# Performance work log

Measured on AMD Instinct MI355X. Metric: run time of the kernel, lower is better.

The kernel has to match this reference:

```python
import jax, jax.numpy as jnp
import numpy as np

EMBED_DIM = 1024
HEADS = 16
HD = EMBED_DIM // HEADS

def setup_inputs() -> dict:
    key = jax.random.key(0)
    ks = jax.random.split(key, 6)
    s = 1.0 / np.sqrt(EMBED_DIM)
    x = jax.random.normal(ks[0], (4, 2048, EMBED_DIM), dtype=jnp.float32)
    Wq = jax.random.uniform(ks[1], (EMBED_DIM, EMBED_DIM), jnp.float32, -s, s)
    Wk = jax.random.uniform(ks[2], (EMBED_DIM, EMBED_DIM), jnp.float32, -s, s)
    Wv = jax.random.uniform(ks[3], (EMBED_DIM, EMBED_DIM), jnp.float32, -s, s)
    Wo = jax.random.uniform(ks[4], (EMBED_DIM, EMBED_DIM), jnp.float32, -s, s)
    bo = jax.random.uniform(ks[5], (EMBED_DIM,), jnp.float32, -s, s)
    return {"x": x, "Wq": Wq, "Wk": Wk, "Wv": Wv, "Wo": Wo, "bo": bo}

def reference(x, Wq, Wk, Wv, Wo, bo):
    B, S, E = x.shape
    # projections (torch Linear: y = x @ W.T), split into heads -> [B,H,S,hd]
    def proj(W):
        return (x @ W.T).reshape(B, S, HEADS, HD).transpose(0, 2, 1, 3)
    q, k, v = proj(Wq), proj(Wk), proj(Wv)
    energy = jnp.einsum('bhid,bhjd->bhij', q, k) / np.sqrt(HD).astype(np.float32)
    causal = jnp.tril(jnp.ones((S, S), dtype=bool))
    energy = jnp.where(causal, energy, -jnp.inf)
    attn = jax.nn.softmax(energy, axis=-1)  # dropout omitted (eval mode)
    out = jnp.einsum('bhij,bhjd->bhid', attn, v)
    out = out.transpose(0, 2, 1, 3).reshape(B, S, E)
    return out @ Wo.T + bo
```

## Files before the change

### kernel.cpp

```cpp
#include <hip/hip_runtime.h>
#include <math.h>

#define EMB   1024
#define HEADS 16
#define HD    64
#define SEQ   2048
#define BATCH 4
#define MTOT  (BATCH * SEQ)
#define XSZ   ((size_t)MTOT * EMB)
#define WSZ   ((size_t)EMB * EMB)

typedef __attribute__((ext_vector_type(8))) short s16x8;
typedef __attribute__((ext_vector_type(4))) short s16x4;
typedef __attribute__((ext_vector_type(4))) float f32x4;

__device__ __forceinline__ short f2bf(float f) {
    unsigned u = __builtin_bit_cast(unsigned, f);
    u += 0x7fffu + ((u >> 16) & 1u);
    return (short)(u >> 16);
}

__device__ __forceinline__ unsigned pk_bf16(float a, float b) {
#if __has_builtin(__builtin_amdgcn_cvt_pk_bf16_f32)
    typedef __attribute__((ext_vector_type(2))) __bf16 bf16x2;
    return __builtin_bit_cast(unsigned, __builtin_amdgcn_cvt_pk_bf16_f32(a, b));
#else
    return (unsigned)(unsigned short)f2bf(a) |
           ((unsigned)(unsigned short)f2bf(b) << 16);
#endif
}

__device__ __forceinline__ float fexp2(float x) {
#if __has_builtin(__builtin_amdgcn_exp2f)
    return __builtin_amdgcn_exp2f(x);
#else
    return exp2f(x);
#endif
}

__device__ __forceinline__ void async16(const void* g, void* l) {
    __builtin_amdgcn_global_load_lds(
        (const __attribute__((address_space(1))) unsigned*)g,
        (__attribute__((address_space(3))) unsigned*)l, 16, 0, 0);
}

__global__ __launch_bounds__(256)
void cvt_inputs(const float* __restrict__ x,  const float* __restrict__ wq,
                const float* __restrict__ wk, const float* __restrict__ wv,
                const float* __restrict__ wo, short* __restrict__ xb,
                short* __restrict__ wcat)
{
    const size_t e = ((size_t)blockIdx.x * 256 + threadIdx.x) * 8;
    const float* src;
    short* dst;
    float scale = 1.0f;
    if (e < XSZ) {
        src = x + e;
        dst = xb + e;
    } else {
        const size_t r = e - XSZ;
        const int w = (int)(r >> 20);
        const size_t off = r & (WSZ - 1);
        src = (w == 0 ? wq : w == 1 ? wk : w == 2 ? wv : wo) + off;
        dst = wcat + r;
        if (w == 0) scale = 0.125f * 1.44269504f;
    }
    const float4 a = ((const float4*)src)[0];
    const float4 b = ((const float4*)src)[1];
    s16x8 v;
    v[0] = f2bf(a.x * scale); v[1] = f2bf(a.y * scale);
    v[2] = f2bf(a.z * scale); v[3] = f2bf(a.w * scale);
    v[4] = f2bf(b.x * scale); v[5] = f2bf(b.y * scale);
    v[6] = f2bf(b.z * scale); v[7] = f2bf(b.w * scale);
    *(s16x8*)dst = v;
}

#define BAR() __builtin_amdgcn_s_barrier()
#define WAIT_LGKM() do { asm volatile("s_waitcnt lgkmcnt(0)" ::: "memory"); \
                         __builtin_amdgcn_sched_barrier(0); } while (0)
#define WAIT_VM(n) asm volatile("s_waitcnt vmcnt(" #n ")" ::: "memory")

#define RD_A4(bA) \
    _Pragma("unroll") for (int mi = 0; mi < 4; ++mi) \
    _Pragma("unroll") for (int kk = 0; kk < 2; ++kk) \
        a[mi][kk] = *(const s16x8*)((bA) + (wm4 + mi) * 2048 + kk * 1024 + abase);

#define RD_B2(bB, hf, breg) \
    _Pragma("unroll") for (int ni = 0; ni < 2; ++ni) \
    _Pragma("unroll") for (int kk = 0; kk < 2; ++kk) \
        breg[ni][kk] = *(const s16x8*)((bB) + (wn4 + (hf) * 2 + ni) * 2048 + kk * 1024 + abase);

#define MFMA16(hf, breg) \
    __builtin_amdgcn_s_setprio(1); \
    _Pragma("unroll") for (int mi = 0; mi < 4; ++mi) \
    _Pragma("unroll") for (int ni = 0; ni < 2; ++ni) \
    _Pragma("unroll") for (int kk = 0; kk < 2; ++kk) \
        acc[mi][(hf) * 2 + ni] = __builtin_amdgcn_mfma_f32_16x16x32_bf16( \
            a[mi][kk], breg[ni][kk], acc[mi][(hf) * 2 + ni], 0, 0, 0); \
    __builtin_amdgcn_s_setprio(0);

#define STA(pM, ldsM, h, k0) do { \
    async16((pM) + (size_t)((h) * 128) * K + (k0),      (ldsM) + (h) * 16384 + wv1024); \
    async16((pM) + (size_t)((h) * 128 + 64) * K + (k0), (ldsM) + (h) * 16384 + 8192 + wv1024); \
} while (0)

#define STB(pM, ldsM, k0) do { \
    async16((pM) + (k0),                (ldsM) + wv1024); \
    async16((pM) + (size_t)64 * K + (k0), (ldsM) + 8192 + wv1024); \
} while (0)

template<bool OUT_BF16>
__global__ __launch_bounds__(512, 2)
void gemm_qp(const short* __restrict__ A, const short* __restrict__ B,
             void* __restrict__ C, int ldc, const float* __restrict__ bias,
             int K)
{
    __shared__ __align__(16) char lds[147456];

    const int tid   = threadIdx.x;
    const int wv    = tid >> 6;
    const int lane  = tid & 63;
    const int col16 = lane & 15;
    const int quad  = lane >> 4;
    const int wm    = wv >> 1;
    const int wn    = wv & 1;
    const int wm4   = wm * 4;
    const int wn4   = wn * 4;
    const int wv1024 = wv << 10;

    const int nwg = gridDim.x * gridDim.y;
    int wg = blockIdx.y * gridDim.x + blockIdx.x;
    wg = (wg & 7) * (nwg >> 3) + (wg >> 3);
    const int rowBase = (wg / gridDim.x) * 256;
    const int colBase = (wg % gridDim.x) * 128;

    const int abase = (col16 * 64 + quad * 16) ^ ((col16 & 8) << 2);

    const int rlane = (lane >> 2) & 15;
    const int rw0   = ((wv >> 1) << 4) + rlane;
    const int colSt = ((wv & 1) << 5) + (((lane & 3) << 3) ^ ((lane & 32) >> 1));
    const short* pA = A + (size_t)(rowBase + rw0) * K + colSt;
    const short* pB = B + (size_t)(colBase + rw0) * K + colSt;

    s16x8 a[4][2], bq0[2][2], bq1[2][2];
    f32x4 acc[4][4];
#pragma unroll
    for (int i = 0; i < 4; ++i)
#pragma unroll
        for (int j = 0; j < 4; ++j) acc[i][j] = (f32x4){0.f, 0.f, 0.f, 0.f};

    const int NT = K >> 6;

    char* r0 = lds;
    char* r1 = lds + 49152;
    char* r2 = lds + 98304;

    STA(pA, r0, 0, 0);  STA(pA, r0, 1, 0);  STB(pB, r0 + 32768, 0);
    STA(pA, r1, 0, 64); STA(pA, r1, 1, 64); STB(pB, r1 + 32768, 64);
    WAIT_VM(6);
    BAR();

    for (int kt = 0; kt < NT; ++kt) {
        const int k0 = kt << 6;
        const bool more = (kt + 2 < NT);

        RD_A4(r0);
        RD_B2(r0 + 32768, 0, bq0);
        if (more) { STA(pA, r2, 0, k0 + 128); STB(pB, r2 + 32768, k0 + 128); }
        BAR(); WAIT_LGKM();
        MFMA16(0, bq0);
        BAR();

        RD_B2(r0 + 32768, 1, bq1);
        if (more) STA(pA, r2, 1, k0 + 128);
        BAR(); WAIT_LGKM();
        MFMA16(1, bq1);
        if (more) { WAIT_VM(6); } else { WAIT_VM(0); }
        BAR();

        char* t = r0; r0 = r1; r1 = r2; r2 = t;
    }

    if (OUT_BF16) {
        short* Cb = (short*)C;
#pragma unroll
        for (int mi = 0; mi < 4; ++mi) {
            const int rg0 = rowBase + wm * 64 + mi * 16 + quad * 4;
#pragma unroll
            for (int ni = 0; ni < 4; ++ni) {
                const int cg = colBase + wn * 64 + ni * 16 + col16;
                const f32x4 v = acc[mi][ni];
#pragma unroll
                for (int r = 0; r < 4; ++r)
                    Cb[(size_t)(rg0 + r) * ldc + cg] = f2bf(v[r]);
            }
        }
    } else {
        float* Cf = (float*)C;
#pragma unroll
        for (int ni = 0; ni < 4; ++ni) {
            const int cg = colBase + wn * 64 + ni * 16 + col16;
            const float bj = bias ? bias[cg] : 0.f;
#pragma unroll
            for (int mi = 0; mi < 4; ++mi) {
                const int rg0 = rowBase + wm * 64 + mi * 16 + quad * 4;
                const f32x4 v = acc[mi][ni];
#pragma unroll
                for (int r = 0; r < 4; ++r)
                    Cf[(size_t)(rg0 + r) * ldc + cg] = v[r] + bj;
            }
        }
    }
}

#define LDQ 3072
__global__ __launch_bounds__(512)
void attn_mfma(const short* __restrict__ QKV, short* __restrict__ O)
{
    __shared__ short lK[64 * 64];
    __shared__ short lV[64 * 64];
    __shared__ short lP[8 * 32 * 64];

    char* lKc = (char*)lK;
    char* lVc = (char*)lV;
    char* lPc = (char*)lP;

    const int tid  = threadIdx.x;
    const int wv   = tid >> 6;
    const int lane = tid & 63;
    const int col  = lane & 15;
    const int quad = lane >> 4;
    const int csw  = (col & 7) << 4;

    const int linear = (int)blockIdx.y * 8 + (int)blockIdx.x;
    const int hlf = linear >> 8;
    const int r9  = linear & 255;
    const int bh  = (hlf << 5) + (r9 >> 3);
    const int xr  = r9 & 7;
    const int qsuper = hlf ? (7 - xr) : xr;

    const int b  = bh >> 4;
    const int h  = bh & 15;
    const size_t baseq = (size_t)b * SEQ * LDQ + (size_t)h * HD;
    const size_t basek = baseq + 1024;
    const size_t basev = baseq + 2048;
    const size_t baseo = (size_t)b * SEQ * EMB + (size_t)h * HD;

    const int krow = tid >> 3;
    const int kwoff = krow * 128 + ((((tid & 7) * 16)) ^ ((krow & 7) << 4));
    char* pwv = lPc + wv * 4096;

    const s16x8 onesv = {0x3F80, 0x3F80, 0x3F80, 0x3F80,
                         0x3F80, 0x3F80, 0x3F80, 0x3F80};

    const int qb = qsuper * 256;
    const int qlo_w = qb + wv * 32;

    s16x8 qf[2][2];
#pragma unroll
    for (int rb = 0; rb < 2; ++rb) {
        const short* qr = QKV + baseq + (size_t)(qlo_w + rb * 16 + col) * LDQ;
        qf[rb][0] = *(const s16x8*)(qr + quad * 8);
        qf[rb][1] = *(const s16x8*)(qr + 32 + quad * 8);
    }

    f32x4 of[2][4], lsum[2];
#pragma unroll
    for (int rb = 0; rb < 2; ++rb) {
#pragma unroll
        for (int u = 0; u < 4; ++u) of[rb][u] = (f32x4){0.f, 0.f, 0.f, 0.f};
        lsum[rb] = (f32x4){0.f, 0.f, 0.f, 0.f};
    }

    const int nt = qb / 64 + 4;

    s16x8 pk = *(const s16x8*)(QKV + basek + (size_t)krow * LDQ + (tid & 7) * 8);
    s16x8 pv = *(const s16x8*)(QKV + basev + (size_t)lane * LDQ + wv * 8);

    for (int kt = 0; kt < nt; ++kt) {
        const int kb = kt * 64;
        __syncthreads();
        *(s16x8*)(lKc + kwoff) = pk;
#pragma unroll
        for (int t = 0; t < 8; ++t)
            *(short*)(lVc + (wv * 8 + t) * 128 + ((lane * 2) ^ (t << 4))) = pv[t];
        __syncthreads();

        if (kt + 1 < nt) {
            pk = *(const s16x8*)(QKV + basek + (size_t)(kb + 64 + krow) * LDQ + (tid & 7) * 8);
            pv = *(const s16x8*)(QKV + basev + (size_t)(kb + 64 + lane) * LDQ + wv * 8);
        }

        if (kb > qlo_w + 31) continue;

        s16x8 kf[4][2];
#pragma unroll
        for (int t = 0; t < 4; ++t) {
            kf[t][0] = *(const s16x8*)(lKc + (t * 16 + col) * 128 + ((quad * 16) ^ csw));
            kf[t][1] = *(const s16x8*)(lKc + (t * 16 + col) * 128 + ((64 + quad * 16) ^ csw));
        }

#pragma unroll
        for (int rb = 0; rb < 2; ++rb) {
            const int qlo = qlo_w + rb * 16;
            const int qg  = qlo + col;

            f32x4 s[4];
#pragma unroll
            for (int t = 0; t < 4; ++t) {
                f32x4 acc = (f32x4){0.f, 0.f, 0.f, 0.f};
                acc = __builtin_amdgcn_mfma_f32_16x16x32_bf16(kf[t][0], qf[rb][0], acc, 0, 0, 0);
                acc = __builtin_amdgcn_mfma_f32_16x16x32_bf16(kf[t][1], qf[rb][1], acc, 0, 0, 0);
                s[t] = acc;
            }

            if (kb + 63 > qlo) {
#pragma unroll
                for (int t = 0; t < 4; ++t)
#pragma unroll
                    for (int rr = 0; rr < 4; ++rr) {
                        const int kg = kb + t * 16 + quad * 4 + rr;
                        if (kg > qg) s[t][rr] = -3.0e38f;
                    }
            }

            char* pb = pwv + (rb * 16 + col) * 128;
#pragma unroll
            for (int t = 0; t < 4; ++t) {
                uint2 pkd;
                pkd.x = pk_bf16(fexp2(s[t][0]), fexp2(s[t][1]));
                pkd.y = pk_bf16(fexp2(s[t][2]), fexp2(s[t][3]));
                *(uint2*)(pb + ((t * 32 + quad * 8) ^ csw)) = pkd;
            }
        }

#pragma unroll
        for (int c = 0; c < 2; ++c) {
            s16x8 vf[4];
#pragma unroll
            for (int u = 0; u < 4; ++u)
                vf[u] = *(const s16x8*)(lVc + (u * 16 + col) * 128 + ((c * 64 + quad * 16) ^ csw));
#pragma unroll
            for (int rb = 0; rb < 2; ++rb) {
                const s16x8 pa = *(const s16x8*)(pwv + (rb * 16 + col) * 128 + ((c * 64 + quad * 16) ^ csw));
                lsum[rb] = __builtin_amdgcn_mfma_f32_16x16x32_bf16(onesv, pa, lsum[rb], 0, 0, 0);
#pragma unroll
                for (int u = 0; u < 4; ++u)
                    of[rb][u] = __builtin_amdgcn_mfma_f32_16x16x32_bf16(vf[u], pa, of[rb][u], 0, 0, 0);
            }
        }
    }

#pragma unroll
    for (int rb = 0; rb < 2; ++rb) {
        const float rl = 1.f / lsum[rb][0];
        short* orow = O + baseo + (size_t)(qlo_w + rb * 16 + col) * EMB + quad * 4;
#pragma unroll
        for (int u = 0; u < 4; ++u) {
            uint2 pkd;
            pkd.x = pk_bf16(of[rb][u][0] * rl, of[rb][u][1] * rl);
            pkd.y = pk_bf16(of[rb][u][2] * rl, of[rb][u][3] * rl);
            *(uint2*)&orow[u * 16] = pkd;
        }
    }
}

extern "C" void kernel_launch(void* const* d_in, const int* in_sizes, int n_in,
                              void* d_out, int out_size, void* d_ws, size_t ws_size,
                              hipStream_t stream)
{
    const float* x  = (const float*)d_in[0];
    const float* Wq = (const float*)d_in[1];
    const float* Wk = (const float*)d_in[2];
    const float* Wv = (const float*)d_in[3];
    const float* Wo = (const float*)d_in[4];
    const float* bo = (const float*)d_in[5];
    float* out = (float*)d_out;

    short* xb   = (short*)d_ws;
    short* wcat = xb + XSZ;
    short* qkv  = wcat + 4 * WSZ;
    short* ob   = qkv + (size_t)MTOT * 3 * EMB;

    const int cvt_blocks = (int)((XSZ + 4 * WSZ) / 8 / 256);
    cvt_inputs<<<cvt_blocks, 256, 0, stream>>>(x, Wq, Wk, Wv, Wo, xb, wcat);

    gemm_qp<true><<<dim3(3072 / 128, MTOT / 256), 512, 0, stream>>>(
        xb, wcat, qkv, 3072, nullptr, EMB);

    attn_mfma<<<dim3(8, BATCH * HEADS), 512, 0, stream>>>(qkv, ob);

    gemm_qp<false><<<dim3(EMB / 128, MTOT / 256), 512, 0, stream>>>(
        ob, wcat + (size_t)3 * WSZ, out, EMB, bo, EMB);
}
```

Measured before the change: 245.5 us.

## Shrink attention blocks to 128 queries with 4 waves, reverse-order scheduling

```diff
diff --git a/kernel.cpp b/kernel.cpp
--- a/kernel.cpp
+++ b/kernel.cpp
@@ -214,12 +214,12 @@
 }
 
 #define LDQ 3072
-__global__ __launch_bounds__(512)
+__global__ __launch_bounds__(256)
 void attn_mfma(const short* __restrict__ QKV, short* __restrict__ O)
 {
     __shared__ short lK[64 * 64];
     __shared__ short lV[64 * 64];
-    __shared__ short lP[8 * 32 * 64];
+    __shared__ short lP[4 * 32 * 64];
 
     char* lKc = (char*)lK;
     char* lVc = (char*)lV;
@@ -232,13 +232,8 @@
     const int quad = lane >> 4;
     const int csw  = (col & 7) << 4;
 
-    const int linear = (int)blockIdx.y * 8 + (int)blockIdx.x;
-    const int hlf = linear >> 8;
-    const int r9  = linear & 255;
-    const int bh  = (hlf << 5) + (r9 >> 3);
-    const int xr  = r9 & 7;
-    const int qsuper = hlf ? (7 - xr) : xr;
-
+    const int qx = 15 - (int)blockIdx.x;
+    const int bh = blockIdx.y;
     const int b  = bh >> 4;
     const int h  = bh & 15;
     const size_t baseq = (size_t)b * SEQ * LDQ + (size_t)h * HD;
@@ -246,14 +241,18 @@
     const size_t basev = baseq + 2048;
     const size_t baseo = (size_t)b * SEQ * EMB + (size_t)h * HD;
 
-    const int krow = tid >> 3;
-    const int kwoff = krow * 128 + ((((tid & 7) * 16)) ^ ((krow & 7) << 4));
+    const int krow = tid >> 2;
+    const int kch  = (tid & 3) * 16;
+    const int ksw  = (krow & 7) << 4;
+    const int vkey = tid & 63;
+    const int vdg  = tid >> 6;
+
     char* pwv = lPc + wv * 4096;
 
     const s16x8 onesv = {0x3F80, 0x3F80, 0x3F80, 0x3F80,
                          0x3F80, 0x3F80, 0x3F80, 0x3F80};
 
-    const int qb = qsuper * 256;
+    const int qb = qx * 128;
     const int qlo_w = qb + wv * 32;
 
     s16x8 qf[2][2];
@@ -272,23 +271,30 @@
         lsum[rb] = (f32x4){0.f, 0.f, 0.f, 0.f};
     }
 
-    const int nt = qb / 64 + 4;
-
-    s16x8 pk = *(const s16x8*)(QKV + basek + (size_t)krow * LDQ + (tid & 7) * 8);
-    s16x8 pv = *(const s16x8*)(QKV + basev + (size_t)lane * LDQ + wv * 8);
+    const int nt = qb / 64 + 2;
+
+    s16x8 pk0 = *(const s16x8*)(QKV + basek + (size_t)krow * LDQ + (tid & 3) * 8);
+    s16x8 pk1 = *(const s16x8*)(QKV + basek + (size_t)krow * LDQ + 32 + (tid & 3) * 8);
+    s16x8 pv0 = *(const s16x8*)(QKV + basev + (size_t)vkey * LDQ + vdg * 16);
+    s16x8 pv1 = *(const s16x8*)(QKV + basev + (size_t)vkey * LDQ + vdg * 16 + 8);
 
     for (int kt = 0; kt < nt; ++kt) {
         const int kb = kt * 64;
         __syncthreads();
-        *(s16x8*)(lKc + kwoff) = pk;
-#pragma unroll
-        for (int t = 0; t < 8; ++t)
-            *(short*)(lVc + (wv * 8 + t) * 128 + ((lane * 2) ^ (t << 4))) = pv[t];
+        *(s16x8*)(lKc + krow * 128 + (kch ^ ksw)) = pk0;
+        *(s16x8*)(lKc + krow * 128 + ((64 + kch) ^ ksw)) = pk1;
+#pragma unroll
+        for (int t = 0; t < 8; ++t) {
+            *(short*)(lVc + (vdg * 16 + t) * 128 + ((vkey * 2) ^ (t << 4))) = pv0[t];
+            *(short*)(lVc + (vdg * 16 + 8 + t) * 128 + ((vkey * 2) ^ (t << 4))) = pv1[t];
+        }
         __syncthreads();
 
         if (kt + 1 < nt) {
-            pk = *(const s16x8*)(QKV + basek + (size_t)(kb + 64 + krow) * LDQ + (tid & 7) * 8);
-            pv = *(const s16x8*)(QKV + basev + (size_t)(kb + 64 + lane) * LDQ + wv * 8);
+            pk0 = *(const s16x8*)(QKV + basek + (size_t)(kb + 64 + krow) * LDQ + (tid & 3) * 8);
+            pk1 = *(const s16x8*)(QKV + basek + (size_t)(kb + 64 + krow) * LDQ + 32 + (tid & 3) * 8);
+            pv0 = *(const s16x8*)(QKV + basev + (size_t)(kb + 64 + vkey) * LDQ + vdg * 16);
+            pv1 = *(const s16x8*)(QKV + basev + (size_t)(kb + 64 + vkey) * LDQ + vdg * 16 + 8);
         }
 
         if (kb > qlo_w + 31) continue;
@@ -388,7 +394,7 @@
     gemm_qp<true><<<dim3(3072 / 128, MTOT / 256), 512, 0, stream>>>(
         xb, wcat, qkv, 3072, nullptr, EMB);
 
-    attn_mfma<<<dim3(8, BATCH * HEADS), 512, 0, stream>>>(qkv, ob);
+    attn_mfma<<<dim3(16, BATCH * HEADS), 256, 0, stream>>>(qkv, ob);
 
     gemm_qp<false><<<dim3(EMB / 128, MTOT / 256), 512, 0, stream>>>(
         ob, wcat + (size_t)3 * WSZ, out, EMB, bo, EMB);
```

Result: slower. 306.0 us (+24.7%).

## Write V transposed from QKV GEMM and pipeline attention K/V loads asynchronously

Applied to the files above, without the earlier changes.

```diff
diff --git a/kernel.cpp b/kernel.cpp
--- a/kernel.cpp
+++ b/kernel.cpp
@@ -113,7 +113,7 @@
 __global__ __launch_bounds__(512, 2)
 void gemm_qp(const short* __restrict__ A, const short* __restrict__ B,
              void* __restrict__ C, int ldc, const float* __restrict__ bias,
-             int K)
+             int K, short* __restrict__ Vt)
 {
     __shared__ __align__(16) char lds[147456];
 
@@ -183,16 +183,36 @@
 
     if (OUT_BF16) {
         short* Cb = (short*)C;
-#pragma unroll
-        for (int mi = 0; mi < 4; ++mi) {
-            const int rg0 = rowBase + wm * 64 + mi * 16 + quad * 4;
-#pragma unroll
-            for (int ni = 0; ni < 4; ++ni) {
-                const int cg = colBase + wn * 64 + ni * 16 + col16;
-                const f32x4 v = acc[mi][ni];
-#pragma unroll
-                for (int r = 0; r < 4; ++r)
-                    Cb[(size_t)(rg0 + r) * ldc + cg] = f2bf(v[r]);
+        if (Vt != nullptr && colBase >= 2048) {
+#pragma unroll
+            for (int mi = 0; mi < 4; ++mi) {
+                const int rg0 = rowBase + wm * 64 + mi * 16 + quad * 4;
+                const int bq = rg0 >> 11;
+                const int s0 = rg0 & 2047;
+#pragma unroll
+                for (int ni = 0; ni < 4; ++ni) {
+                    const int cg2 = colBase - 2048 + wn * 64 + ni * 16 + col16;
+                    const int hh = cg2 >> 6, dd = cg2 & 63;
+                    short* dst = Vt + (((size_t)(bq * 16 + hh) * 64 + dd) << 11) + s0;
+                    const f32x4 v = acc[mi][ni];
+                    uint2 pw;
+                    pw.x = pk_bf16(v[0], v[1]);
+                    pw.y = pk_bf16(v[2], v[3]);
+                    *(uint2*)dst = pw;
+                }
+            }
+        } else {
+#pragma unroll
+            for (int mi = 0; mi < 4; ++mi) {
+                const int rg0 = rowBase + wm * 64 + mi * 16 + quad * 4;
+#pragma unroll
+                for (int ni = 0; ni < 4; ++ni) {
+                    const int cg = colBase + wn * 64 + ni * 16 + col16;
+                    const f32x4 v = acc[mi][ni];
+#pragma unroll
+                    for (int r = 0; r < 4; ++r)
+                        Cb[(size_t)(rg0 + r) * ldc + cg] = f2bf(v[r]);
+                }
             }
         }
     } else {
@@ -213,16 +233,14 @@
     }
 }
 
-#define LDQ 3072
+#define LDT 2048
 __global__ __launch_bounds__(512)
-void attn_mfma(const short* __restrict__ QKV, short* __restrict__ O)
+void attn_mfma(const short* __restrict__ QK, const short* __restrict__ VT,
+               short* __restrict__ O)
 {
-    __shared__ short lK[64 * 64];
-    __shared__ short lV[64 * 64];
+    __shared__ __align__(16) short lKV[4][2][64 * 64];
     __shared__ short lP[8 * 32 * 64];
 
-    char* lKc = (char*)lK;
-    char* lVc = (char*)lV;
     char* lPc = (char*)lP;
 
     const int tid  = threadIdx.x;
@@ -232,137 +250,143 @@
     const int quad = lane >> 4;
     const int csw  = (col & 7) << 4;
 
-    const int linear = (int)blockIdx.y * 8 + (int)blockIdx.x;
-    const int hlf = linear >> 8;
-    const int r9  = linear & 255;
-    const int bh  = (hlf << 5) + (r9 >> 3);
-    const int xr  = r9 & 7;
-    const int qsuper = hlf ? (7 - xr) : xr;
-
+    const int bh = blockIdx.y;
     const int b  = bh >> 4;
     const int h  = bh & 15;
-    const size_t baseq = (size_t)b * SEQ * LDQ + (size_t)h * HD;
+    const size_t baseq = (size_t)b * SEQ * LDT + (size_t)h * HD;
     const size_t basek = baseq + 1024;
-    const size_t basev = baseq + 2048;
     const size_t baseo = (size_t)b * SEQ * EMB + (size_t)h * HD;
-
-    const int krow = tid >> 3;
-    const int kwoff = krow * 128 + ((((tid & 7) * 16)) ^ ((krow & 7) << 4));
+    const short* vtb = VT + ((size_t)bh << 17);
+
+    const int srow   = tid >> 3;
+    const int schunk = tid & 7;
+    const int ssc    = (schunk ^ (srow & 7)) * 8;
+    const int sdst   = srow * 128 + schunk * 16;
+
     char* pwv = lPc + wv * 4096;
 
     const s16x8 onesv = {0x3F80, 0x3F80, 0x3F80, 0x3F80,
                          0x3F80, 0x3F80, 0x3F80, 0x3F80};
 
-    const int qb = qsuper * 256;
-    const int qlo_w = qb + wv * 32;
-
-    s16x8 qf[2][2];
-#pragma unroll
-    for (int rb = 0; rb < 2; ++rb) {
-        const short* qr = QKV + baseq + (size_t)(qlo_w + rb * 16 + col) * LDQ;
-        qf[rb][0] = *(const s16x8*)(qr + quad * 8);
-        qf[rb][1] = *(const s16x8*)(qr + 32 + quad * 8);
+#define STG(kt, bi) do { \
+    async16(QK + basek + (size_t)((kt) * 64 + srow) * LDT + ssc, (char*)lKV[bi][0] + sdst); \
+    async16(vtb + (size_t)srow * LDT + (kt) * 64 + ssc,          (char*)lKV[bi][1] + sdst); \
+} while (0)
+
+    for (int half = 0; half < 2; ++half) {
+        const int qsuper = half ? (7 - (int)blockIdx.x) : (int)blockIdx.x;
+        const int qb = qsuper * 256;
+        const int qlo_w = qb + wv * 32;
+
+        s16x8 qf[2][2];
+#pragma unroll
+        for (int rb = 0; rb < 2; ++rb) {
+            const short* qr = QK + baseq + (size_t)(qlo_w + rb * 16 + col) * LDT;
+            qf[rb][0] = *(const s16x8*)(qr + quad * 8);
+            qf[rb][1] = *(const s16x8*)(qr + 32 + quad * 8);
+        }
+
+        f32x4 of[2][4], lsum[2];
+#pragma unroll
+        for (int rb = 0; rb < 2; ++rb) {
+#pragma unroll
+            for (int u = 0; u < 4; ++u) of[rb][u] = (f32x4){0.f, 0.f, 0.f, 0.f};
+            lsum[rb] = (f32x4){0.f, 0.f, 0.f, 0.f};
+        }
+
+        const int nt = qb / 64 + 4;
+
+        BAR();
+        STG(0, 0);
+        STG(1, 1);
+
+        for (int kt = 0; kt < nt; ++kt) {
+            const int kb = kt * 64;
+            const int bi = kt & 3;
+            if (kt + 2 < nt) STG(kt + 2, (kt + 2) & 3);
+            const int rem = nt - 1 - kt;
+            if (rem >= 2)      { WAIT_VM(4); }
+            else if (rem == 1) { WAIT_VM(2); }
+            else               { WAIT_VM(0); }
+            BAR();
+
+            if (kb > qlo_w + 31) continue;
+
+            const char* lKb = (const char*)lKV[bi][0];
+            const char* lVb = (const char*)lKV[bi][1];
+
+            s16x8 kf[4][2];
+#pragma unroll
+            for (int t = 0; t < 4; ++t) {
+                kf[t][0] = *(const s16x8*)(lKb + (t * 16 + col) * 128 + ((quad * 16) ^ csw));
+                kf[t][1] = *(const s16x8*)(lKb + (t * 16 + col) * 128 + ((64 + quad * 16) ^ csw));
+            }
+
+#pragma unroll
+            for (int rb = 0; rb < 2; ++rb) {
+                const int qlo = qlo_w + rb * 16;
+                const int qg  = qlo + col;
+
+                f32x4 s[4];
+#pragma unroll
+                for (int t = 0; t < 4; ++t) {
+                    f32x4 acc = (f32x4){0.f, 0.f, 0.f, 0.f};
+                    acc = __builtin_amdgcn_mfma_f32_16x16x32_bf16(kf[t][0], qf[rb][0], acc, 0, 0, 0);
+                    acc = __builtin_amdgcn_mfma_f32_16x16x32_bf16(kf[t][1], qf[rb][1], acc, 0, 0, 0);
+                    s[t] = acc;
+                }
+
+                if (kb + 63 > qlo) {
+#pragma unroll
+                    for (int t = 0; t < 4; ++t)
+#pragma unroll
+                        for (int rr = 0; rr < 4; ++rr) {
+                            const int kg = kb + t * 16 + quad * 4 + rr;
+                            if (kg > qg) s[t][rr] = -3.0e38f;
+                        }
+                }
+
+                char* pb = pwv + (rb * 16 + col) * 128;
+#pragma unroll
+                for (int t = 0; t < 4; ++t) {
+                    uint2 pkd;
+                    pkd.x = pk_bf16(fexp2(s[t][0]), fexp2(s[t][1]));
+                    pkd.y = pk_bf16(fexp2(s[t][2]), fexp2(s[t][3]));
+                    *(uint2*)(pb + ((t * 32 + quad * 8) ^ csw)) = pkd;
+                }
+            }
+
+#pragma unroll
+            for (int c = 0; c < 2; ++c) {
+                s16x8 vf[4];
+#pragma unroll
+                for (int u = 0; u < 4; ++u)
+                    vf[u] = *(const s16x8*)(lVb + (u * 16 + col) * 128 + ((c * 64 + quad * 16) ^ csw));
+#pragma unroll
+                for (int rb = 0; rb < 2; ++rb) {
+                    const s16x8 pa = *(const s16x8*)(pwv + (rb * 16 + col) * 128 + ((c * 64 + quad * 16) ^ csw));
+                    lsum[rb] = __builtin_amdgcn_mfma_f32_16x16x32_bf16(onesv, pa, lsum[rb], 0, 0, 0);
+#pragma unroll
+                    for (int u = 0; u < 4; ++u)
+                        of[rb][u] = __builtin_amdgcn_mfma_f32_16x16x32_bf16(vf[u], pa, of[rb][u], 0, 0, 0);
+                }
+            }
+        }
+
+#pragma unroll
+        for (int rb = 0; rb < 2; ++rb) {
+            const float rl = 1.f / lsum[rb][0];
+            short* orow = O + baseo + (size_t)(qlo_w + rb * 16 + col) * EMB + quad * 4;
+#pragma unroll
+            for (int u = 0; u < 4; ++u) {
+                uint2 pkd;
+                pkd.x = pk_bf16(of[rb][u][0] * rl, of[rb][u][1] * rl);
+                pkd.y = pk_bf16(of[rb][u][2] * rl, of[rb][u][3] * rl);
+                *(uint2*)&orow[u * 16] = pkd;
+            }
+        }
     }
-
-    f32x4 of[2][4], lsum[2];
-#pragma unroll
-    for (int rb = 0; rb < 2; ++rb) {
-#pragma unroll
-        for (int u = 0; u < 4; ++u) of[rb][u] = (f32x4){0.f, 0.f, 0.f, 0.f};
-        lsum[rb] = (f32x4){0.f, 0.f, 0.f, 0.f};
-    }
-
-    const int nt = qb / 64 + 4;
-
-    s16x8 pk = *(const s16x8*)(QKV + basek + (size_t)krow * LDQ + (tid & 7) * 8);
-    s16x8 pv = *(const s16x8*)(QKV + basev + (size_t)lane * LDQ + wv * 8);
-
-    for (int kt = 0; kt < nt; ++kt) {
-        const int kb = kt * 64;
-        __syncthreads();
-        *(s16x8*)(lKc + kwoff) = pk;
-#pragma unroll
-        for (int t = 0; t < 8; ++t)
-            *(short*)(lVc + (wv * 8 + t) * 128 + ((lane * 2) ^ (t << 4))) = pv[t];
-        __syncthreads();
-
-        if (kt + 1 < nt) {
-            pk = *(const s16x8*)(QKV + basek + (size_t)(kb + 64 + krow) * LDQ + (tid & 7) * 8);
-            pv = *(const s16x8*)(QKV + basev + (size_t)(kb + 64 + lane) * LDQ + wv * 8);
-        }
-
-        if (kb > qlo_w + 31) continue;
-
-        s16x8 kf[4][2];
-#pragma unroll
-        for (int t = 0; t < 4; ++t) {
-            kf[t][0] = *(const s16x8*)(lKc + (t * 16 + col) * 128 + ((quad * 16) ^ csw));
-            kf[t][1] = *(const s16x8*)(lKc + (t * 16 + col) * 128 + ((64 + quad * 16) ^ csw));
-        }
-
-#pragma unroll
-        for (int rb = 0; rb < 2; ++rb) {
-            const int qlo = qlo_w + rb * 16;
-            const int qg  = qlo + col;
-
-            f32x4 s[4];
-#pragma unroll
-            for (int t = 0; t < 4; ++t) {
-                f32x4 acc = (f32x4){0.f, 0.f, 0.f, 0.f};
-                acc = __builtin_amdgcn_mfma_f32_16x16x32_bf16(kf[t][0], qf[rb][0], acc, 0, 0, 0);
-                acc = __builtin_amdgcn_mfma_f32_16x16x32_bf16(kf[t][1], qf[rb][1], acc, 0, 0, 0);
-                s[t] = acc;
-            }
-
-            if (kb + 63 > qlo) {
-#pragma unroll
-                for (int t = 0; t < 4; ++t)
-#pragma unroll
-                    for (int rr = 0; rr < 4; ++rr) {
-                        const int kg = kb + t * 16 + quad * 4 + rr;
-                        if (kg > qg) s[t][rr] = -3.0e38f;
-                    }
-            }
-
-            char* pb = pwv + (rb * 16 + col) * 128;
-#pragma unroll
-            for (int t = 0; t < 4; ++t) {
-                uint2 pkd;
-                pkd.x = pk_bf16(fexp2(s[t][0]), fexp2(s[t][1]));
-                pkd.y = pk_bf16(fexp2(s[t][2]), fexp2(s[t][3]));
-                *(uint2*)(pb + ((t * 32 + quad * 8) ^ csw)) = pkd;
-            }
-        }
-
-#pragma unroll
-        for (int c = 0; c < 2; ++c) {
-            s16x8 vf[4];
-#pragma unroll
-            for (int u = 0; u < 4; ++u)
-                vf[u] = *(const s16x8*)(lVc + (u * 16 + col) * 128 + ((c * 64 + quad * 16) ^ csw));
-#pragma unroll
-            for (int rb = 0; rb < 2; ++rb) {
-                const s16x8 pa = *(const s16x8*)(pwv + (rb * 16 + col) * 128 + ((c * 64 + quad * 16) ^ csw));
-                lsum[rb] = __builtin_amdgcn_mfma_f32_16x16x32_bf16(onesv, pa, lsum[rb], 0, 0, 0);
-#pragma unroll
-                for (int u = 0; u < 4; ++u)
-                    of[rb][u] = __builtin_amdgcn_mfma_f32_16x16x32_bf16(vf[u], pa, of[rb][u], 0, 0, 0);
-            }
-        }
-    }
-
-#pragma unroll
-    for (int rb = 0; rb < 2; ++rb) {
-        const float rl = 1.f / lsum[rb][0];
-        short* orow = O + baseo + (size_t)(qlo_w + rb * 16 + col) * EMB + quad * 4;
-#pragma unroll
-        for (int u = 0; u < 4; ++u) {
-            uint2 pkd;
-            pkd.x = pk_bf16(of[rb][u][0] * rl, of[rb][u][1] * rl);
-            pkd.y = pk_bf16(of[rb][u][2] * rl, of[rb][u][3] * rl);
-            *(uint2*)&orow[u * 16] = pkd;
-        }
-    }
+#undef STG
 }
 
 extern "C" void kernel_launch(void* const* d_in, const int* in_sizes, int n_in,
@@ -379,17 +403,18 @@
 
     short* xb   = (short*)d_ws;
     short* wcat = xb + XSZ;
-    short* qkv  = wcat + 4 * WSZ;
-    short* ob   = qkv + (size_t)MTOT * 3 * EMB;
+    short* qk   = wcat + 4 * WSZ;
+    short* vt   = qk + (size_t)MTOT * 2048;
+    short* ob   = vt + (size_t)64 * 64 * 2048;
 
     const int cvt_blocks = (int)((XSZ + 4 * WSZ) / 8 / 256);
     cvt_inputs<<<cvt_blocks, 256, 0, stream>>>(x, Wq, Wk, Wv, Wo, xb, wcat);
 
     gemm_qp<true><<<dim3(3072 / 128, MTOT / 256), 512, 0, stream>>>(
-        xb, wcat, qkv, 3072, nullptr, EMB);
-
-    attn_mfma<<<dim3(8, BATCH * HEADS), 512, 0, stream>>>(qkv, ob);
+        xb, wcat, qk, 2048, nullptr, EMB, vt);
+
+    attn_mfma<<<dim3(4, BATCH * HEADS), 512, 0, stream>>>(qk, vt, ob);
 
     gemm_qp<false><<<dim3(EMB / 128, MTOT / 256), 512, 0, stream>>>(
-        ob, wcat + (size_t)3 * WSZ, out, EMB, bo, EMB);
-}
+        ob, wcat + (size_t)3 * WSZ, out, EMB, bo, EMB, nullptr);
+}
```

Result: no change. 243.9 us (-0.6%).
